# Optimization experiments

Measured on AMD Instinct MI355X. Metric: run time of the kernel, lower is better.

## Reference

```python
import jax, jax.numpy as jnp
import numpy as np

IOU_THRESH = 0.6
NEG = -1.0  # strictly below any real IoU (IoU >= 0), used to mask cross-label pairs


def cxcywh_to_xyxy(b):
    cx, cy, w, h = b[..., 0], b[..., 1], b[..., 2], b[..., 3]
    return jnp.stack([cx - 0.5 * w, cy - 0.5 * h, cx + 0.5 * w, cy + 0.5 * h], axis=-1)


def pairwise_iou(a, b):
    # a: [M,4] xyxy, b: [N,4] xyxy -> [M,N]
    area_a = (a[:, 2] - a[:, 0]) * (a[:, 3] - a[:, 1])
    area_b = (b[:, 2] - b[:, 0]) * (b[:, 3] - b[:, 1])
    lt = jnp.maximum(a[:, None, :2], b[None, :, :2])
    rb = jnp.minimum(a[:, None, 2:], b[None, :, 2:])
    wh = jnp.clip(rb - lt, 0.0, None)
    inter = wh[..., 0] * wh[..., 1]
    union = area_a[:, None] + area_b[None, :] - inter
    return inter / jnp.maximum(union, 1e-9)


def assign_one(proposals, prompt_inds, gt_boxes, gt_labels, k):
    # Vectorized equivalent of the per-unique-label loop: masking IoU to NEG for
    # cross-label (gt, proposal) pairs reproduces the per-group matcher exactly.
    M = gt_boxes.shape[0]
    match = gt_labels[:, None] == prompt_inds[None, :]                # [M,N] group membership
    iou = pairwise_iou(cxcywh_to_xyxy(gt_boxes), cxcywh_to_xyxy(proposals))  # [M,N]
    miou = jnp.where(match, iou, NEG)                                 # group-masked IoU
    best_iou = miou.max(axis=0)                                       # [N] matcher argmax within group
    best_gt = miou.argmax(axis=0)
    valid_prop = match.any(axis=0)                                    # proposal's label appears in gt
    gmax = miou.max(axis=1)                                           # [M] per-gt best IoU in its group
    lq = (miou == gmax[:, None]) & match                              # allow_low_quality_matches
    pos = valid_prop & ((best_iou >= IOU_THRESH) | lq.any(axis=0))    # matched_labels == 1 (foreground)
    # positives assigned to each gt (fg cap num_queries*0.25 never binds at these sizes)
    counts = jax.ops.segment_sum(pos.astype(jnp.int32), best_gt, num_segments=M)
    # sample_topk_per_gt: per gt take top min(count, k) proposals by group IoU
    topv, topi = jax.lax.top_k(miou, k)                               # [M,k]
    take = jnp.minimum(counts, k)
    valid = jnp.arange(k)[None, :] < take[:, None]                    # [M,k]
    rows = jnp.where(valid, topi, -1)                                 # proposal indices, -1 padded
    cols = jnp.where(valid, jnp.arange(M)[:, None], -1)               # gt indices, -1 padded
    sel_iou = jnp.where(valid, topv, 0.0)
    return rows, cols, valid, sel_iou


def setup_inputs() -> dict:
    key = jax.random.key(0)
    ks = jax.random.split(key, 6)
    B, N, M, L = 16, 3000, 300, 80

    def boxes(k, shape):
        u = jax.random.uniform(k, shape + (4,), dtype=jnp.float32)
        cxcy = u[..., :2]
        wh = 0.02 + 0.28 * u[..., 2:]  # cxcywh with positive extents
        return jnp.concatenate([cxcy, wh], axis=-1)

    return {
        "pred_logits_match": jax.random.normal(ks[0], (B, N, 1), dtype=jnp.float32),
        "pred_boxes": boxes(ks[1], (B, N)),
        "init_reference": boxes(ks[2], (B, N)),
        "prompt_inds": jax.random.randint(ks[3], (B, N), 0, L, dtype=jnp.int32),
        "gt_labels": jax.random.randint(ks[4], (B, M), 0, L, dtype=jnp.int32),
        "gt_boxes": boxes(ks[5], (B, M)),
        "max_k": 4,
    }


def reference(pred_logits_match, pred_boxes, init_reference, prompt_inds, gt_labels, gt_boxes, max_k):
    _ = jax.nn.sigmoid(pred_logits_match)  # computed in the original forward but unused downstream
    f = lambda p, pi, gb, gl: assign_one(p, pi, gb, gl, max_k)
    rows, cols, valid, sel_iou = jax.vmap(f)(init_reference, prompt_inds, gt_boxes, gt_labels)
    # padded equivalent of the list of (rows, cols) index pairs; valid marks real entries
    return rows, cols, valid, sel_iou
```

## Files before the change

### kernel.cpp

```cpp
#include <hip/hip_runtime.h>

#define BB 16
#define NN 3000
#define MM 300
#define LL 80
#define KK 4
#define IOU_THRESH 0.6f

typedef unsigned long long u64;

struct Box { float x1, y1, x2, y2, area; };

__device__ __forceinline__ Box to_xyxy(float4 b) {
#pragma clang fp contract(off)
    Box r;
    r.x1 = b.x - 0.5f * b.z;
    r.y1 = b.y - 0.5f * b.w;
    r.x2 = b.x + 0.5f * b.z;
    r.y2 = b.y + 0.5f * b.w;
    r.area = (r.x2 - r.x1) * (r.y2 - r.y1);
    return r;
}

__device__ __forceinline__ float pair_iou(Box a, Box b) {
#pragma clang fp contract(off)
    float ltx = fmaxf(a.x1, b.x1);
    float lty = fmaxf(a.y1, b.y1);
    float rbx = fminf(a.x2, b.x2);
    float rby = fminf(a.y2, b.y2);
    float wx = fmaxf(rbx - ltx, 0.0f);
    float wy = fmaxf(rby - lty, 0.0f);
    float inter = wx * wy;
    float uni = a.area + b.area - inter;
    return inter / fmaxf(uni, 1e-9f);
}

__device__ __forceinline__ unsigned int f32_to_ordered(float f) {
    unsigned int u = __float_as_uint(f);
    return (u & 0x80000000u) ? ~u : (u | 0x80000000u);
}
__device__ __forceinline__ float ordered_to_f32(unsigned int u) {
    unsigned int b = (u & 0x80000000u) ? (u & 0x7FFFFFFFu) : ~u;
    return __uint_as_float(b);
}

__device__ __forceinline__ u64 umax64(u64 a, u64 b) { return a > b ? a : b; }
__device__ __forceinline__ u64 umin64(u64 a, u64 b) { return a < b ? a : b; }

__device__ __forceinline__ u64 shfl_xor_u64(u64 v, int mask) {
    int lo = __shfl_xor((int)(unsigned)v, mask, 64);
    int hi = __shfl_xor((int)(unsigned)(v >> 32), mask, 64);
    return ((u64)(unsigned)hi << 32) | (u64)(unsigned)lo;
}

__device__ __forceinline__ void topins(u64 t[4], u64 k) {
    u64 c0 = umin64(t[0], k);
    t[0] = umax64(t[0], k);
    u64 c1 = umin64(t[1], c0);
    t[1] = umax64(t[1], c0);
    u64 c2 = umin64(t[2], c1);
    t[2] = umax64(t[2], c1);
    t[3] = umax64(t[3], c2);
}

__device__ __forceinline__ void wave_merge_top4(u64 t[4]) {
    #pragma unroll
    for (int s = 1; s < 64; s <<= 1) {
        u64 b0 = shfl_xor_u64(t[0], s);
        u64 b1 = shfl_xor_u64(t[1], s);
        u64 b2 = shfl_xor_u64(t[2], s);
        u64 b3 = shfl_xor_u64(t[3], s);
        u64 a0 = t[0], a1 = t[1], a2 = t[2], a3 = t[3];
        t[0] = umax64(a0, b0);
        t[1] = umax64(umin64(a0, b0), umax64(a1, b1));
        t[2] = umax64(umax64(a2, b2), umax64(umin64(a0, b1), umin64(a1, b0)));
        t[3] = umax64(umax64(a3, b3),
               umax64(umin64(a0, b2), umax64(umin64(a1, b1), umin64(a2, b0))));
    }
}

__global__ __launch_bounds__(256) void kBin(const int* __restrict__ pinds,
                                            const int* __restrict__ glab,
                                            unsigned short* __restrict__ pidx,
                                            int* __restrict__ pstart,
                                            int* __restrict__ pcnt,
                                            unsigned short* __restrict__ gidx,
                                            int* __restrict__ gstart,
                                            int* __restrict__ gcnt,
                                            int* __restrict__ counts) {
    int b = blockIdx.x;
    int tid = threadIdx.x;
    __shared__ int hist[LL], cur[LL], gh[LL], gcur[LL];
    if (tid < LL) { hist[tid] = 0; gh[tid] = 0; }
    __syncthreads();
    for (int n = tid; n < NN; n += 256) atomicAdd(&hist[pinds[b * NN + n]], 1);
    for (int m = tid; m < MM; m += 256) atomicAdd(&gh[glab[b * MM + m]], 1);
    __syncthreads();
    if (tid < LL) {
        int s = 0;
        for (int j = 0; j < tid; ++j) s += hist[j];
        cur[tid] = s; pstart[b * LL + tid] = s; pcnt[b * LL + tid] = hist[tid];
        int t = 0;
        for (int j = 0; j < tid; ++j) t += gh[j];
        gcur[tid] = t; gstart[b * LL + tid] = t; gcnt[b * LL + tid] = gh[tid];
    }
    __syncthreads();
    for (int n = tid; n < NN; n += 256) {
        int l = pinds[b * NN + n];
        int pos = atomicAdd(&cur[l], 1);
        pidx[b * NN + pos] = (unsigned short)n;
    }
    for (int m = tid; m < MM; m += 256) {
        int l = glab[b * MM + m];
        int pos = atomicAdd(&gcur[l], 1);
        gidx[b * MM + pos] = (unsigned short)m;
    }
    for (int i = tid; i < MM; i += 256) counts[b * MM + i] = 0;
}

__global__ __launch_bounds__(256) void kTop(const float4* __restrict__ props,
                                            const int*    __restrict__ glab,
                                            const float4* __restrict__ gbox,
                                            const unsigned short* __restrict__ pidx,
                                            const int* __restrict__ pstart,
                                            const int* __restrict__ pcnt,
                                            const unsigned short* __restrict__ gidx,
                                            float* out) {
    int b = blockIdx.y;
    int wv = __builtin_amdgcn_readfirstlane((int)(threadIdx.x >> 6));
    int lane = threadIdx.x & 63;
    int g = blockIdx.x * 4 + wv;
    int m = gidx[b * MM + g];
    int bm = b * MM + m;
    Box gt = to_xyxy(gbox[bm]);
    int l = glab[bm];
    int s = pstart[b * LL + l], c = pcnt[b * LL + l];

    const u64 init = ((u64)f32_to_ordered(-1.0f) << 32);
    u64 t[4] = {init, init, init, init};
    for (int i = lane; i < c; i += 64) {
        int n = pidx[b * NN + s + i];
        Box pb = to_xyxy(props[(size_t)b * NN + n]);
        float iou = pair_iou(gt, pb);
        u64 key = ((u64)f32_to_ordered(iou) << 32) |
                  (u64)(0xFFFFFFFFu - (unsigned)n);
        topins(t, key);
    }
    wave_merge_top4(t);

    if (lane == 0) {
        float* topv = out + 38400;
        int*   topi = (int*)(out + 57600);
        #pragma unroll
        for (int j = 0; j < KK; ++j) {
            topv[bm * KK + j] = ordered_to_f32((unsigned)(t[j] >> 32));
            topi[bm * KK + j] = (int)(0xFFFFFFFFu - (unsigned)t[j]);
        }
        float gm = ordered_to_f32((unsigned)(t[0] >> 32));
        float4* gtb = (float4*)out;
        int gpos = b * MM + g;
        gtb[gpos * 2 + 0] = make_float4(gt.x1, gt.y1, gt.x2, gt.y2);
        gtb[gpos * 2 + 1] = make_float4(gt.area, gm, __int_as_float(m), 0.0f);
    }
}

__global__ __launch_bounds__(256) void kAsn(const float4* __restrict__ props,
                                            const int*    __restrict__ pinds,
                                            const int* __restrict__ gstart,
                                            const int* __restrict__ gcnt,
                                            const float* __restrict__ out,
                                            int* __restrict__ counts) {
    int b = blockIdx.y;
    int n = blockIdx.x * 256 + threadIdx.x;
    if (n >= NN) return;
    float4 pr = props[(size_t)b * NN + n];
    int lbl = pinds[(size_t)b * NN + n];
    Box pb = to_xyxy(pr);
    int s = gstart[b * LL + lbl], c = gcnt[b * LL + lbl];
    const float4* gtb = (const float4*)out;

    u64 key = 0;
    bool lq = false;
    for (int j = 0; j < c; ++j) {
        int idx = (b * MM + s + j) * 2;
        float4 q0 = gtb[idx], q1 = gtb[idx + 1];
        Box a; a.x1 = q0.x; a.y1 = q0.y; a.x2 = q0.z; a.y2 = q0.w; a.area = q1.x;
        float iou = pair_iou(a, pb);
        int m = __float_as_int(q1.z);
        u64 k = ((u64)f32_to_ordered(iou) << 32) |
                (u64)(0xFFFFFFFFu - (unsigned)m);
        key = umax64(key, k);
        lq = lq || (iou == q1.y);
    }
    if (c > 0) {
        float v = ordered_to_f32((unsigned)(key >> 32));
        int bm = (int)(0xFFFFFFFFu - (unsigned)key);
        if ((v >= IOU_THRESH) || lq) atomicAdd(&counts[b * MM + bm], 1);
    }
}

__global__ __launch_bounds__(256) void kC(const int* __restrict__ counts,
                                          float* out) {
    int i = blockIdx.x * 256 + threadIdx.x;
    if (i >= BB * MM) return;
    int m = i % MM;
    int take = min(counts[i], KK);
    float4 tv = ((const float4*)(out + 38400))[i];
    int4   ti = ((const int4*)(out + 57600))[i];
    float4 rows, cols, valid, sel;
    rows.x = (0 < take) ? (float)ti.x : -1.0f;
    rows.y = (1 < take) ? (float)ti.y : -1.0f;
    rows.z = (2 < take) ? (float)ti.z : -1.0f;
    rows.w = (3 < take) ? (float)ti.w : -1.0f;
    cols.x = (0 < take) ? (float)m : -1.0f;
    cols.y = (1 < take) ? (float)m : -1.0f;
    cols.z = (2 < take) ? (float)m : -1.0f;
    cols.w = (3 < take) ? (float)m : -1.0f;
    valid.x = (0 < take) ? 1.0f : 0.0f;
    valid.y = (1 < take) ? 1.0f : 0.0f;
    valid.z = (2 < take) ? 1.0f : 0.0f;
    valid.w = (3 < take) ? 1.0f : 0.0f;
    sel.x = (0 < take) ? tv.x : 0.0f;
    sel.y = (1 < take) ? tv.y : 0.0f;
    sel.z = (2 < take) ? tv.z : 0.0f;
    sel.w = (3 < take) ? tv.w : 0.0f;
    float4* o = (float4*)out;
    const int CH4 = BB * MM;
    o[0 * CH4 + i] = rows;
    o[1 * CH4 + i] = cols;
    o[2 * CH4 + i] = valid;
    o[3 * CH4 + i] = sel;
}

extern "C" void kernel_launch(void* const* d_in, const int* in_sizes, int n_in,
                              void* d_out, int out_size, void* d_ws, size_t ws_size,
                              hipStream_t stream) {
    const float4* props = (const float4*)d_in[2];
    const int*    pinds = (const int*)d_in[3];
    const int*    glab  = (const int*)d_in[4];
    const float4* gbox  = (const float4*)d_in[5];
    float* out = (float*)d_out;

    char* w = (char*)d_ws;
    int*   counts = (int*)w;                 w += BB * MM * sizeof(int);
    int*   pstart = (int*)w;                 w += BB * LL * sizeof(int);
    int*   pcnt   = (int*)w;                 w += BB * LL * sizeof(int);
    int*   gstart = (int*)w;                 w += BB * LL * sizeof(int);
    int*   gcnt   = (int*)w;                 w += BB * LL * sizeof(int);
    unsigned short* pidx = (unsigned short*)w; w += BB * NN * sizeof(short);
    unsigned short* gidx = (unsigned short*)w;

    kBin<<<BB, 256, 0, stream>>>(pinds, glab, pidx, pstart, pcnt,
                                 gidx, gstart, gcnt, counts);
    dim3 gT(MM / 4, BB);
    kTop<<<gT, 256, 0, stream>>>(props, glab, gbox, pidx, pstart, pcnt, gidx, out);
    dim3 gA((NN + 255) / 256, BB);
    kAsn<<<gA, 256, 0, stream>>>(props, pinds, gstart, gcnt, out, counts);
    kC<<<(BB * MM + 255) / 256, 256, 0, stream>>>(counts, out);
}
```

Baseline: 89.76 us.

## Fuse top-k, assignment and output kernels into persistent kernel with grid barriers

Replaces the kTop, kAsn and kC launches with one persistent kernel of 512 blocks that moves between phases through a software grid barrier built on agent-scope atomics. The binning kernel is split across 32 blocks, proposal binning and gt binning in separate blocks, so each block does less serial work. It also resets the barrier counters and zeroes counts. The aim is to cut kernel launch and inter-kernel gap overhead. The risks are barrier spin cost and deadlock if all 512 blocks cannot be resident at once, which the code relies on through launch_bounds(256,2).

```diff
diff --git a/kernel.cpp b/kernel.cpp
--- a/kernel.cpp
+++ b/kernel.cpp
@@ -6,6 +6,7 @@
 #define LL 80
 #define KK 4
 #define IOU_THRESH 0.6f
+#define GRID 512
 
 typedef unsigned long long u64;
 
@@ -79,157 +80,202 @@
     }
 }
 
-__global__ __launch_bounds__(256) void kBin(const int* __restrict__ pinds,
-                                            const int* __restrict__ glab,
-                                            unsigned short* __restrict__ pidx,
-                                            int* __restrict__ pstart,
-                                            int* __restrict__ pcnt,
-                                            unsigned short* __restrict__ gidx,
-                                            int* __restrict__ gstart,
-                                            int* __restrict__ gcnt,
-                                            int* __restrict__ counts) {
-    int b = blockIdx.x;
+__device__ __forceinline__ void grid_barrier(unsigned* cnt, unsigned* gen) {
+    __syncthreads();
+    if (threadIdx.x == 0) {
+        __threadfence();
+        unsigned g = __hip_atomic_load(gen, __ATOMIC_ACQUIRE, __HIP_MEMORY_SCOPE_AGENT);
+        unsigned a = __hip_atomic_fetch_add(cnt, 1u, __ATOMIC_ACQ_REL, __HIP_MEMORY_SCOPE_AGENT);
+        if (a == GRID - 1) {
+            __hip_atomic_store(cnt, 0u, __ATOMIC_RELAXED, __HIP_MEMORY_SCOPE_AGENT);
+            __hip_atomic_store(gen, g + 1u, __ATOMIC_RELEASE, __HIP_MEMORY_SCOPE_AGENT);
+        } else {
+            while (__hip_atomic_load(gen, __ATOMIC_ACQUIRE, __HIP_MEMORY_SCOPE_AGENT) == g) {
+                __builtin_amdgcn_s_sleep(1);
+            }
+        }
+        __threadfence();
+    }
+    __syncthreads();
+}
+
+__global__ __launch_bounds__(256) void kPrep(const int* __restrict__ pinds,
+                                             const int* __restrict__ glab,
+                                             unsigned short* __restrict__ pidx,
+                                             int* __restrict__ pstart,
+                                             int* __restrict__ pcnt,
+                                             unsigned short* __restrict__ gidx,
+                                             int* __restrict__ gstart,
+                                             int* __restrict__ gcnt,
+                                             int* __restrict__ counts,
+                                             unsigned* __restrict__ bar) {
+    int blk = blockIdx.x;
     int tid = threadIdx.x;
-    __shared__ int hist[LL], cur[LL], gh[LL], gcur[LL];
-    if (tid < LL) { hist[tid] = 0; gh[tid] = 0; }
-    __syncthreads();
-    for (int n = tid; n < NN; n += 256) atomicAdd(&hist[pinds[b * NN + n]], 1);
-    for (int m = tid; m < MM; m += 256) atomicAdd(&gh[glab[b * MM + m]], 1);
-    __syncthreads();
-    if (tid < LL) {
-        int s = 0;
-        for (int j = 0; j < tid; ++j) s += hist[j];
-        cur[tid] = s; pstart[b * LL + tid] = s; pcnt[b * LL + tid] = hist[tid];
-        int t = 0;
-        for (int j = 0; j < tid; ++j) t += gh[j];
-        gcur[tid] = t; gstart[b * LL + tid] = t; gcnt[b * LL + tid] = gh[tid];
-    }
-    __syncthreads();
-    for (int n = tid; n < NN; n += 256) {
-        int l = pinds[b * NN + n];
-        int pos = atomicAdd(&cur[l], 1);
-        pidx[b * NN + pos] = (unsigned short)n;
-    }
-    for (int m = tid; m < MM; m += 256) {
-        int l = glab[b * MM + m];
-        int pos = atomicAdd(&gcur[l], 1);
-        gidx[b * MM + pos] = (unsigned short)m;
-    }
-    for (int i = tid; i < MM; i += 256) counts[b * MM + i] = 0;
-}
-
-__global__ __launch_bounds__(256) void kTop(const float4* __restrict__ props,
-                                            const int*    __restrict__ glab,
-                                            const float4* __restrict__ gbox,
-                                            const unsigned short* __restrict__ pidx,
-                                            const int* __restrict__ pstart,
-                                            const int* __restrict__ pcnt,
-                                            const unsigned short* __restrict__ gidx,
-                                            float* out) {
-    int b = blockIdx.y;
-    int wv = __builtin_amdgcn_readfirstlane((int)(threadIdx.x >> 6));
-    int lane = threadIdx.x & 63;
-    int g = blockIdx.x * 4 + wv;
-    int m = gidx[b * MM + g];
-    int bm = b * MM + m;
-    Box gt = to_xyxy(gbox[bm]);
-    int l = glab[bm];
-    int s = pstart[b * LL + l], c = pcnt[b * LL + l];
-
-    const u64 init = ((u64)f32_to_ordered(-1.0f) << 32);
-    u64 t[4] = {init, init, init, init};
-    for (int i = lane; i < c; i += 64) {
-        int n = pidx[b * NN + s + i];
-        Box pb = to_xyxy(props[(size_t)b * NN + n]);
-        float iou = pair_iou(gt, pb);
-        u64 key = ((u64)f32_to_ordered(iou) << 32) |
-                  (u64)(0xFFFFFFFFu - (unsigned)n);
-        topins(t, key);
-    }
-    wave_merge_top4(t);
-
-    if (lane == 0) {
+    __shared__ int hist[LL], cur[LL];
+
+    if (blk == 0 && tid == 0) { bar[0] = 0u; bar[1] = 0u; }
+
+    for (int i = blk * 256 + tid; i < BB * MM; i += 32 * 256) counts[i] = 0;
+
+    if (blk < BB) {
+        int b = blk;
+        if (tid < LL) hist[tid] = 0;
+        __syncthreads();
+        for (int n = tid; n < NN; n += 256) atomicAdd(&hist[pinds[b * NN + n]], 1);
+        __syncthreads();
+        if (tid < LL) {
+            int s = 0;
+            for (int j = 0; j < tid; ++j) s += hist[j];
+            cur[tid] = s; pstart[b * LL + tid] = s; pcnt[b * LL + tid] = hist[tid];
+        }
+        __syncthreads();
+        for (int n = tid; n < NN; n += 256) {
+            int l = pinds[b * NN + n];
+            int pos = atomicAdd(&cur[l], 1);
+            pidx[b * NN + pos] = (unsigned short)n;
+        }
+    } else {
+        int b = blk - BB;
+        if (tid < LL) hist[tid] = 0;
+        __syncthreads();
+        for (int m = tid; m < MM; m += 256) atomicAdd(&hist[glab[b * MM + m]], 1);
+        __syncthreads();
+        if (tid < LL) {
+            int s = 0;
+            for (int j = 0; j < tid; ++j) s += hist[j];
+            cur[tid] = s; gstart[b * LL + tid] = s; gcnt[b * LL + tid] = hist[tid];
+        }
+        __syncthreads();
+        for (int m = tid; m < MM; m += 256) {
+            int l = glab[b * MM + m];
+            int pos = atomicAdd(&cur[l], 1);
+            gidx[b * MM + pos] = (unsigned short)m;
+        }
+    }
+}
+
+__global__ __launch_bounds__(256, 2) void kMain(
+    const float4* __restrict__ props, const int* __restrict__ pinds,
+    const int* __restrict__ glab, const float4* __restrict__ gbox,
+    float* __restrict__ out, int* __restrict__ counts,
+    const int* __restrict__ pstart, const int* __restrict__ pcnt,
+    const int* __restrict__ gstart, const int* __restrict__ gcnt,
+    const unsigned short* __restrict__ pidx, const unsigned short* __restrict__ gidx,
+    unsigned* __restrict__ bar)
+{
+    const int tid = threadIdx.x;
+    const int blk = blockIdx.x;
+
+    {
+        const int lane = tid & 63;
+        const int wv = (blk << 2) + (tid >> 6);
+        const int nw = GRID << 2;
         float* topv = out + 38400;
         int*   topi = (int*)(out + 57600);
-        #pragma unroll
-        for (int j = 0; j < KK; ++j) {
-            topv[bm * KK + j] = ordered_to_f32((unsigned)(t[j] >> 32));
-            topi[bm * KK + j] = (int)(0xFFFFFFFFu - (unsigned)t[j]);
-        }
-        float gm = ordered_to_f32((unsigned)(t[0] >> 32));
         float4* gtb = (float4*)out;
-        int gpos = b * MM + g;
-        gtb[gpos * 2 + 0] = make_float4(gt.x1, gt.y1, gt.x2, gt.y2);
-        gtb[gpos * 2 + 1] = make_float4(gt.area, gm, __int_as_float(m), 0.0f);
-    }
-}
-
-__global__ __launch_bounds__(256) void kAsn(const float4* __restrict__ props,
-                                            const int*    __restrict__ pinds,
-                                            const int* __restrict__ gstart,
-                                            const int* __restrict__ gcnt,
-                                            const float* __restrict__ out,
-                                            int* __restrict__ counts) {
-    int b = blockIdx.y;
-    int n = blockIdx.x * 256 + threadIdx.x;
-    if (n >= NN) return;
-    float4 pr = props[(size_t)b * NN + n];
-    int lbl = pinds[(size_t)b * NN + n];
-    Box pb = to_xyxy(pr);
-    int s = gstart[b * LL + lbl], c = gcnt[b * LL + lbl];
-    const float4* gtb = (const float4*)out;
-
-    u64 key = 0;
-    bool lq = false;
-    for (int j = 0; j < c; ++j) {
-        int idx = (b * MM + s + j) * 2;
-        float4 q0 = gtb[idx], q1 = gtb[idx + 1];
-        Box a; a.x1 = q0.x; a.y1 = q0.y; a.x2 = q0.z; a.y2 = q0.w; a.area = q1.x;
-        float iou = pair_iou(a, pb);
-        int m = __float_as_int(q1.z);
-        u64 k = ((u64)f32_to_ordered(iou) << 32) |
-                (u64)(0xFFFFFFFFu - (unsigned)m);
-        key = umax64(key, k);
-        lq = lq || (iou == q1.y);
-    }
-    if (c > 0) {
-        float v = ordered_to_f32((unsigned)(key >> 32));
-        int bm = (int)(0xFFFFFFFFu - (unsigned)key);
-        if ((v >= IOU_THRESH) || lq) atomicAdd(&counts[b * MM + bm], 1);
-    }
-}
-
-__global__ __launch_bounds__(256) void kC(const int* __restrict__ counts,
-                                          float* out) {
-    int i = blockIdx.x * 256 + threadIdx.x;
-    if (i >= BB * MM) return;
-    int m = i % MM;
-    int take = min(counts[i], KK);
-    float4 tv = ((const float4*)(out + 38400))[i];
-    int4   ti = ((const int4*)(out + 57600))[i];
-    float4 rows, cols, valid, sel;
-    rows.x = (0 < take) ? (float)ti.x : -1.0f;
-    rows.y = (1 < take) ? (float)ti.y : -1.0f;
-    rows.z = (2 < take) ? (float)ti.z : -1.0f;
-    rows.w = (3 < take) ? (float)ti.w : -1.0f;
-    cols.x = (0 < take) ? (float)m : -1.0f;
-    cols.y = (1 < take) ? (float)m : -1.0f;
-    cols.z = (2 < take) ? (float)m : -1.0f;
-    cols.w = (3 < take) ? (float)m : -1.0f;
-    valid.x = (0 < take) ? 1.0f : 0.0f;
-    valid.y = (1 < take) ? 1.0f : 0.0f;
-    valid.z = (2 < take) ? 1.0f : 0.0f;
-    valid.w = (3 < take) ? 1.0f : 0.0f;
-    sel.x = (0 < take) ? tv.x : 0.0f;
-    sel.y = (1 < take) ? tv.y : 0.0f;
-    sel.z = (2 < take) ? tv.z : 0.0f;
-    sel.w = (3 < take) ? tv.w : 0.0f;
-    float4* o = (float4*)out;
-    const int CH4 = BB * MM;
-    o[0 * CH4 + i] = rows;
-    o[1 * CH4 + i] = cols;
-    o[2 * CH4 + i] = valid;
-    o[3 * CH4 + i] = sel;
+        for (int task = wv; task < BB * MM; task += nw) {
+            int tt = __builtin_amdgcn_readfirstlane(task);
+            int b = tt / MM, g = tt - b * MM;
+            int m = gidx[b * MM + g];
+            int bm = b * MM + m;
+            Box gt = to_xyxy(gbox[bm]);
+            int l = glab[bm];
+            int s = pstart[b * LL + l], c = pcnt[b * LL + l];
+
+            const u64 init = ((u64)f32_to_ordered(-1.0f) << 32);
+            u64 t[4] = {init, init, init, init};
+            for (int i = lane; i < c; i += 64) {
+                int n = pidx[b * NN + s + i];
+                Box pb = to_xyxy(props[(size_t)b * NN + n]);
+                float iou = pair_iou(gt, pb);
+                u64 key = ((u64)f32_to_ordered(iou) << 32) |
+                          (u64)(0xFFFFFFFFu - (unsigned)n);
+                topins(t, key);
+            }
+            wave_merge_top4(t);
+
+            if (lane == 0) {
+                #pragma unroll
+                for (int j = 0; j < KK; ++j) {
+                    topv[bm * KK + j] = ordered_to_f32((unsigned)(t[j] >> 32));
+                    topi[bm * KK + j] = (int)(0xFFFFFFFFu - (unsigned)t[j]);
+                }
+                float gm = ordered_to_f32((unsigned)(t[0] >> 32));
+                int gpos = b * MM + g;
+                gtb[gpos * 2 + 0] = make_float4(gt.x1, gt.y1, gt.x2, gt.y2);
+                gtb[gpos * 2 + 1] = make_float4(gt.area, gm, __int_as_float(m), 0.0f);
+            }
+        }
+    }
+
+    grid_barrier(bar, bar + 1);
+
+    {
+        const int gtid = blk * 256 + tid;
+        const int gsz = GRID * 256;
+        const float4* gtb = (const float4*)out;
+        for (int i = gtid; i < BB * NN; i += gsz) {
+            int b = i / NN;
+            float4 pr = props[i];
+            int lbl = pinds[i];
+            Box pb = to_xyxy(pr);
+            int s = gstart[b * LL + lbl], c = gcnt[b * LL + lbl];
+
+            u64 key = 0;
+            bool lq = false;
+            for (int j = 0; j < c; ++j) {
+                int idx = (b * MM + s + j) * 2;
+                float4 q0 = gtb[idx], q1 = gtb[idx + 1];
+                Box a; a.x1 = q0.x; a.y1 = q0.y; a.x2 = q0.z; a.y2 = q0.w; a.area = q1.x;
+                float iou = pair_iou(a, pb);
+                int m = __float_as_int(q1.z);
+                u64 k = ((u64)f32_to_ordered(iou) << 32) |
+                        (u64)(0xFFFFFFFFu - (unsigned)m);
+                key = umax64(key, k);
+                lq = lq || (iou == q1.y);
+            }
+            if (c > 0) {
+                float v = ordered_to_f32((unsigned)(key >> 32));
+                int bm = (int)(0xFFFFFFFFu - (unsigned)key);
+                if ((v >= IOU_THRESH) || lq) atomicAdd(&counts[b * MM + bm], 1);
+            }
+        }
+    }
+
+    grid_barrier(bar, bar + 1);
+
+    {
+        const int gtid = blk * 256 + tid;
+        for (int i = gtid; i < BB * MM; i += GRID * 256) {
+            int m = i % MM;
+            int take = min(counts[i], KK);
+            float4 tv = ((const float4*)(out + 38400))[i];
+            int4   ti = ((const int4*)(out + 57600))[i];
+            float4 rows, cols, valid, sel;
+            rows.x = (0 < take) ? (float)ti.x : -1.0f;
+            rows.y = (1 < take) ? (float)ti.y : -1.0f;
+            rows.z = (2 < take) ? (float)ti.z : -1.0f;
+            rows.w = (3 < take) ? (float)ti.w : -1.0f;
+            cols.x = (0 < take) ? (float)m : -1.0f;
+            cols.y = (1 < take) ? (float)m : -1.0f;
+            cols.z = (2 < take) ? (float)m : -1.0f;
+            cols.w = (3 < take) ? (float)m : -1.0f;
+            valid.x = (0 < take) ? 1.0f : 0.0f;
+            valid.y = (1 < take) ? 1.0f : 0.0f;
+            valid.z = (2 < take) ? 1.0f : 0.0f;
+            valid.w = (3 < take) ? 1.0f : 0.0f;
+            sel.x = (0 < take) ? tv.x : 0.0f;
+            sel.y = (1 < take) ? tv.y : 0.0f;
+            sel.z = (2 < take) ? tv.z : 0.0f;
+            sel.w = (3 < take) ? tv.w : 0.0f;
+            float4* o = (float4*)out;
+            const int CH4 = BB * MM;
+            o[0 * CH4 + i] = rows;
+            o[1 * CH4 + i] = cols;
+            o[2 * CH4 + i] = valid;
+            o[3 * CH4 + i] = sel;
+        }
+    }
 }
 
 extern "C" void kernel_launch(void* const* d_in, const int* in_sizes, int n_in,
@@ -248,13 +294,11 @@
     int*   gstart = (int*)w;                 w += BB * LL * sizeof(int);
     int*   gcnt   = (int*)w;                 w += BB * LL * sizeof(int);
     unsigned short* pidx = (unsigned short*)w; w += BB * NN * sizeof(short);
-    unsigned short* gidx = (unsigned short*)w;
-
-    kBin<<<BB, 256, 0, stream>>>(pinds, glab, pidx, pstart, pcnt,
-                                 gidx, gstart, gcnt, counts);
-    dim3 gT(MM / 4, BB);
-    kTop<<<gT, 256, 0, stream>>>(props, glab, gbox, pidx, pstart, pcnt, gidx, out);
-    dim3 gA((NN + 255) / 256, BB);
-    kAsn<<<gA, 256, 0, stream>>>(props, pinds, gstart, gcnt, out, counts);
-    kC<<<(BB * MM + 255) / 256, 256, 0, stream>>>(counts, out);
-}
+    unsigned short* gidx = (unsigned short*)w; w += BB * MM * sizeof(short);
+    unsigned* bar = (unsigned*)w;
+
+    kPrep<<<32, 256, 0, stream>>>(pinds, glab, pidx, pstart, pcnt,
+                                  gidx, gstart, gcnt, counts, bar);
+    kMain<<<GRID, 256, 0, stream>>>(props, pinds, glab, gbox, out, counts,
+                                    pstart, pcnt, gstart, gcnt, pidx, gidx, bar);
+}
```

Result: slower. 263.4 us (+193.4%).

## Fuse four kernels into one per-(label,batch) block with shared-memory binning

Applied to the files above, without the earlier changes.

Replaces the four kernels (binning, per-gt top-k, per-proposal assignment, finalize) with a single kernel that launches one block per (label, batch). Each block gathers its label's proposals and gts into shared memory, computes the per-gt top-4, assigns proposals and counts positives in shared memory, then writes the outputs. This removes three launches, the global workspace round-trips and the global atomics. In exchange, each block scans all 3000 proposal labels to build its own list, which is redundant work across the 80 label blocks. Parallelism within a block is limited by the small per-label group sizes.

```diff
diff --git a/kernel.cpp b/kernel.cpp
--- a/kernel.cpp
+++ b/kernel.cpp
@@ -79,157 +79,123 @@
     }
 }
 
-__global__ __launch_bounds__(256) void kBin(const int* __restrict__ pinds,
-                                            const int* __restrict__ glab,
-                                            unsigned short* __restrict__ pidx,
-                                            int* __restrict__ pstart,
-                                            int* __restrict__ pcnt,
-                                            unsigned short* __restrict__ gidx,
-                                            int* __restrict__ gstart,
-                                            int* __restrict__ gcnt,
-                                            int* __restrict__ counts) {
-    int b = blockIdx.x;
-    int tid = threadIdx.x;
-    __shared__ int hist[LL], cur[LL], gh[LL], gcur[LL];
-    if (tid < LL) { hist[tid] = 0; gh[tid] = 0; }
-    __syncthreads();
-    for (int n = tid; n < NN; n += 256) atomicAdd(&hist[pinds[b * NN + n]], 1);
-    for (int m = tid; m < MM; m += 256) atomicAdd(&gh[glab[b * MM + m]], 1);
-    __syncthreads();
-    if (tid < LL) {
-        int s = 0;
-        for (int j = 0; j < tid; ++j) s += hist[j];
-        cur[tid] = s; pstart[b * LL + tid] = s; pcnt[b * LL + tid] = hist[tid];
-        int t = 0;
-        for (int j = 0; j < tid; ++j) t += gh[j];
-        gcur[tid] = t; gstart[b * LL + tid] = t; gcnt[b * LL + tid] = gh[tid];
-    }
-    __syncthreads();
+__global__ __launch_bounds__(256) void kFused(
+    const float4* __restrict__ props, const int* __restrict__ pinds,
+    const int* __restrict__ glab, const float4* __restrict__ gbox,
+    float* __restrict__ out)
+{
+    const int l = blockIdx.x;
+    const int b = blockIdx.y;
+    const int tid = threadIdx.x;
+
+    __shared__ unsigned short plist[NN];
+    __shared__ unsigned short glist[MM];
+    __shared__ float gmaxL[MM];
+    __shared__ float tvL[MM * KK];
+    __shared__ int   tiL[MM * KK];
+    __shared__ int   cntsL[MM];
+    __shared__ int pcur, gcur;
+
+    if (tid == 0) { pcur = 0; gcur = 0; }
+    for (int j = tid; j < MM; j += 256) cntsL[j] = 0;
+    __syncthreads();
+
+    for (int m = tid; m < MM; m += 256) {
+        if (glab[b * MM + m] == l) {
+            int pos = atomicAdd(&gcur, 1);
+            glist[pos] = (unsigned short)m;
+        }
+    }
+    __syncthreads();
+    const int cg_ = gcur;
+    if (cg_ == 0) return;
+
     for (int n = tid; n < NN; n += 256) {
-        int l = pinds[b * NN + n];
-        int pos = atomicAdd(&cur[l], 1);
-        pidx[b * NN + pos] = (unsigned short)n;
-    }
-    for (int m = tid; m < MM; m += 256) {
-        int l = glab[b * MM + m];
-        int pos = atomicAdd(&gcur[l], 1);
-        gidx[b * MM + pos] = (unsigned short)m;
-    }
-    for (int i = tid; i < MM; i += 256) counts[b * MM + i] = 0;
-}
-
-__global__ __launch_bounds__(256) void kTop(const float4* __restrict__ props,
-                                            const int*    __restrict__ glab,
-                                            const float4* __restrict__ gbox,
-                                            const unsigned short* __restrict__ pidx,
-                                            const int* __restrict__ pstart,
-                                            const int* __restrict__ pcnt,
-                                            const unsigned short* __restrict__ gidx,
-                                            float* out) {
-    int b = blockIdx.y;
-    int wv = __builtin_amdgcn_readfirstlane((int)(threadIdx.x >> 6));
-    int lane = threadIdx.x & 63;
-    int g = blockIdx.x * 4 + wv;
-    int m = gidx[b * MM + g];
-    int bm = b * MM + m;
-    Box gt = to_xyxy(gbox[bm]);
-    int l = glab[bm];
-    int s = pstart[b * LL + l], c = pcnt[b * LL + l];
-
-    const u64 init = ((u64)f32_to_ordered(-1.0f) << 32);
-    u64 t[4] = {init, init, init, init};
-    for (int i = lane; i < c; i += 64) {
-        int n = pidx[b * NN + s + i];
+        if (pinds[b * NN + n] == l) {
+            int pos = atomicAdd(&pcur, 1);
+            plist[pos] = (unsigned short)n;
+        }
+    }
+    __syncthreads();
+    const int cp_ = pcur;
+
+    {
+        const int lane = tid & 63;
+        const int wv = tid >> 6;
+        for (int j = wv; j < cg_; j += 4) {
+            int m = glist[j];
+            Box gt = to_xyxy(gbox[b * MM + m]);
+            const u64 init = ((u64)f32_to_ordered(-1.0f) << 32);
+            u64 t[4] = {init, init, init, init};
+            for (int i = lane; i < cp_; i += 64) {
+                int n = plist[i];
+                Box pb = to_xyxy(props[(size_t)b * NN + n]);
+                float iou = pair_iou(gt, pb);
+                u64 key = ((u64)f32_to_ordered(iou) << 32) |
+                          (u64)(0xFFFFFFFFu - (unsigned)n);
+                topins(t, key);
+            }
+            wave_merge_top4(t);
+            if (lane == 0) {
+                #pragma unroll
+                for (int q = 0; q < KK; ++q) {
+                    tvL[j * KK + q] = ordered_to_f32((unsigned)(t[q] >> 32));
+                    tiL[j * KK + q] = (int)(0xFFFFFFFFu - (unsigned)t[q]);
+                }
+                gmaxL[j] = ordered_to_f32((unsigned)(t[0] >> 32));
+            }
+        }
+    }
+    __syncthreads();
+
+    for (int p = tid; p < cp_; p += 256) {
+        int n = plist[p];
         Box pb = to_xyxy(props[(size_t)b * NN + n]);
-        float iou = pair_iou(gt, pb);
-        u64 key = ((u64)f32_to_ordered(iou) << 32) |
-                  (u64)(0xFFFFFFFFu - (unsigned)n);
-        topins(t, key);
-    }
-    wave_merge_top4(t);
-
-    if (lane == 0) {
-        float* topv = out + 38400;
-        int*   topi = (int*)(out + 57600);
-        #pragma unroll
-        for (int j = 0; j < KK; ++j) {
-            topv[bm * KK + j] = ordered_to_f32((unsigned)(t[j] >> 32));
-            topi[bm * KK + j] = (int)(0xFFFFFFFFu - (unsigned)t[j]);
-        }
-        float gm = ordered_to_f32((unsigned)(t[0] >> 32));
-        float4* gtb = (float4*)out;
-        int gpos = b * MM + g;
-        gtb[gpos * 2 + 0] = make_float4(gt.x1, gt.y1, gt.x2, gt.y2);
-        gtb[gpos * 2 + 1] = make_float4(gt.area, gm, __int_as_float(m), 0.0f);
-    }
-}
-
-__global__ __launch_bounds__(256) void kAsn(const float4* __restrict__ props,
-                                            const int*    __restrict__ pinds,
-                                            const int* __restrict__ gstart,
-                                            const int* __restrict__ gcnt,
-                                            const float* __restrict__ out,
-                                            int* __restrict__ counts) {
-    int b = blockIdx.y;
-    int n = blockIdx.x * 256 + threadIdx.x;
-    if (n >= NN) return;
-    float4 pr = props[(size_t)b * NN + n];
-    int lbl = pinds[(size_t)b * NN + n];
-    Box pb = to_xyxy(pr);
-    int s = gstart[b * LL + lbl], c = gcnt[b * LL + lbl];
-    const float4* gtb = (const float4*)out;
-
-    u64 key = 0;
-    bool lq = false;
-    for (int j = 0; j < c; ++j) {
-        int idx = (b * MM + s + j) * 2;
-        float4 q0 = gtb[idx], q1 = gtb[idx + 1];
-        Box a; a.x1 = q0.x; a.y1 = q0.y; a.x2 = q0.z; a.y2 = q0.w; a.area = q1.x;
-        float iou = pair_iou(a, pb);
-        int m = __float_as_int(q1.z);
-        u64 k = ((u64)f32_to_ordered(iou) << 32) |
-                (u64)(0xFFFFFFFFu - (unsigned)m);
-        key = umax64(key, k);
-        lq = lq || (iou == q1.y);
-    }
-    if (c > 0) {
+        u64 key = 0;
+        int bestj = 0;
+        bool lq = false;
+        for (int j = 0; j < cg_; ++j) {
+            int m = glist[j];
+            Box gt = to_xyxy(gbox[b * MM + m]);
+            float iou = pair_iou(gt, pb);
+            u64 k = ((u64)f32_to_ordered(iou) << 32) |
+                    (u64)(0xFFFFFFFFu - (unsigned)m);
+            if (k > key) { key = k; bestj = j; }
+            lq = lq || (iou == gmaxL[j]);
+        }
         float v = ordered_to_f32((unsigned)(key >> 32));
-        int bm = (int)(0xFFFFFFFFu - (unsigned)key);
-        if ((v >= IOU_THRESH) || lq) atomicAdd(&counts[b * MM + bm], 1);
-    }
-}
-
-__global__ __launch_bounds__(256) void kC(const int* __restrict__ counts,
-                                          float* out) {
-    int i = blockIdx.x * 256 + threadIdx.x;
-    if (i >= BB * MM) return;
-    int m = i % MM;
-    int take = min(counts[i], KK);
-    float4 tv = ((const float4*)(out + 38400))[i];
-    int4   ti = ((const int4*)(out + 57600))[i];
-    float4 rows, cols, valid, sel;
-    rows.x = (0 < take) ? (float)ti.x : -1.0f;
-    rows.y = (1 < take) ? (float)ti.y : -1.0f;
-    rows.z = (2 < take) ? (float)ti.z : -1.0f;
-    rows.w = (3 < take) ? (float)ti.w : -1.0f;
-    cols.x = (0 < take) ? (float)m : -1.0f;
-    cols.y = (1 < take) ? (float)m : -1.0f;
-    cols.z = (2 < take) ? (float)m : -1.0f;
-    cols.w = (3 < take) ? (float)m : -1.0f;
-    valid.x = (0 < take) ? 1.0f : 0.0f;
-    valid.y = (1 < take) ? 1.0f : 0.0f;
-    valid.z = (2 < take) ? 1.0f : 0.0f;
-    valid.w = (3 < take) ? 1.0f : 0.0f;
-    sel.x = (0 < take) ? tv.x : 0.0f;
-    sel.y = (1 < take) ? tv.y : 0.0f;
-    sel.z = (2 < take) ? tv.z : 0.0f;
-    sel.w = (3 < take) ? tv.w : 0.0f;
-    float4* o = (float4*)out;
-    const int CH4 = BB * MM;
-    o[0 * CH4 + i] = rows;
-    o[1 * CH4 + i] = cols;
-    o[2 * CH4 + i] = valid;
-    o[3 * CH4 + i] = sel;
+        if ((v >= IOU_THRESH) || lq) atomicAdd(&cntsL[bestj], 1);
+    }
+    __syncthreads();
+
+    for (int j = tid; j < cg_; j += 256) {
+        int m = glist[j];
+        int i = b * MM + m;
+        int take = min(cntsL[j], KK);
+        float4 rows, cols, valid, sel;
+        rows.x = (0 < take) ? (float)tiL[j * KK + 0] : -1.0f;
+        rows.y = (1 < take) ? (float)tiL[j * KK + 1] : -1.0f;
+        rows.z = (2 < take) ? (float)tiL[j * KK + 2] : -1.0f;
+        rows.w = (3 < take) ? (float)tiL[j * KK + 3] : -1.0f;
+        cols.x = (0 < take) ? (float)m : -1.0f;
+        cols.y = (1 < take) ? (float)m : -1.0f;
+        cols.z = (2 < take) ? (float)m : -1.0f;
+        cols.w = (3 < take) ? (float)m : -1.0f;
+        valid.x = (0 < take) ? 1.0f : 0.0f;
+        valid.y = (1 < take) ? 1.0f : 0.0f;
+        valid.z = (2 < take) ? 1.0f : 0.0f;
+        valid.w = (3 < take) ? 1.0f : 0.0f;
+        sel.x = (0 < take) ? tvL[j * KK + 0] : 0.0f;
+        sel.y = (1 < take) ? tvL[j * KK + 1] : 0.0f;
+        sel.z = (2 < take) ? tvL[j * KK + 2] : 0.0f;
+        sel.w = (3 < take) ? tvL[j * KK + 3] : 0.0f;
+        float4* o = (float4*)out;
+        const int CH4 = BB * MM;
+        o[0 * CH4 + i] = rows;
+        o[1 * CH4 + i] = cols;
+        o[2 * CH4 + i] = valid;
+        o[3 * CH4 + i] = sel;
+    }
 }
 
 extern "C" void kernel_launch(void* const* d_in, const int* in_sizes, int n_in,
@@ -241,20 +207,5 @@
     const float4* gbox  = (const float4*)d_in[5];
     float* out = (float*)d_out;
 
-    char* w = (char*)d_ws;
-    int*   counts = (int*)w;                 w += BB * MM * sizeof(int);
-    int*   pstart = (int*)w;                 w += BB * LL * sizeof(int);
-    int*   pcnt   = (int*)w;                 w += BB * LL * sizeof(int);
-    int*   gstart = (int*)w;                 w += BB * LL * sizeof(int);
-    int*   gcnt   = (int*)w;                 w += BB * LL * sizeof(int);
-    unsigned short* pidx = (unsigned short*)w; w += BB * NN * sizeof(short);
-    unsigned short* gidx = (unsigned short*)w;
-
-    kBin<<<BB, 256, 0, stream>>>(pinds, glab, pidx, pstart, pcnt,
-                                 gidx, gstart, gcnt, counts);
-    dim3 gT(MM / 4, BB);
-    kTop<<<gT, 256, 0, stream>>>(props, glab, gbox, pidx, pstart, pcnt, gidx, out);
-    dim3 gA((NN + 255) / 256, BB);
-    kAsn<<<gA, 256, 0, stream>>>(props, pinds, gstart, gcnt, out, counts);
-    kC<<<(BB * MM + 255) / 256, 256, 0, stream>>>(counts, out);
-}
+    kFused<<<dim3(LL, BB), 256, 0, stream>>>(props, pinds, glab, gbox, out);
+}
```

Measured after the change: 81.06 us. -9.7%, faster.
